# Kernel tuning notes

Hardware: AMD Instinct MI355X
Metric: run time of the kernel (lower is better)

Reference implementation:

```python
import jax, jax.numpy as jnp
import numpy as np


def table_operator(A, B):
    # A, B: (size, batch). Returns (16, size, batch) of soft logic-gate outputs.
    AB = A * B
    A_or_B = A + B - AB
    A_xor_B = A + B - 2.0 * AB
    return jnp.stack([
        jnp.zeros_like(A),          # 0: FALSE
        AB,                         # 1: A AND B
        A - AB,                     # 2: A AND NOT B
        A,                          # 3: A
        B - AB,                     # 4: NOT A AND B
        B,                          # 5: B
        A_xor_B,                    # 6: A XOR B
        A_or_B,                     # 7: A OR B
        1.0 - A_or_B,               # 8: NOR
        1.0 - A_xor_B,              # 9: XNOR
        1.0 - B,                    # 10: NOT B
        1.0 - B + AB,               # 11: B -> A
        1.0 - A,                    # 12: NOT A
        1.0 - A + AB,               # 13: A -> B
        1.0 - AB,                   # 14: NAND
        jnp.ones_like(A),           # 15: TRUE
    ], axis=0)


def setup_inputs() -> dict:
    key = jax.random.key(0)
    k1, k2, k3, k4 = jax.random.split(key, 4)
    prev_size, size, batch = 1024, 1024, 16384
    return {
        "prev_layer_output": jax.random.uniform(k1, (prev_size, batch), jnp.float32),
        "input_A_weights": jax.random.normal(k2, (size, prev_size), jnp.float32),
        "input_B_weights": jax.random.normal(k3, (size, prev_size), jnp.float32),
        "table_weights": jax.random.normal(k4, (16, size), jnp.float32),
    }


def reference(prev_layer_output, input_A_weights, input_B_weights, table_weights):
    # Inference path (torch.is_grad_enabled() == False, drop_out_rate == 0):
    # plain softmaxes, no multiplier shift, no dropout. GradFactor is identity in fwd.
    pA = jax.nn.softmax(input_A_weights, axis=1)   # (size, prev_size)
    pB = jax.nn.softmax(input_B_weights, axis=1)
    pT = jax.nn.softmax(table_weights, axis=0)     # (16, size)
    a = pA @ prev_layer_output                     # (size, batch)
    b = pB @ prev_layer_output                     # (size, batch)
    gates = table_operator(a, b)                   # (16, size, batch)
    return jnp.sum(gates * pT[:, :, None], axis=0)  # (size, batch)
```

## Files before the change

### kernel.cpp

```cpp
#include <hip/hip_runtime.h>
#include <hip/hip_bf16.h>


typedef __attribute__((ext_vector_type(8))) short bf16x8;
typedef __attribute__((ext_vector_type(4))) float f32x4;

__device__ __forceinline__ void gload_lds16(const void* g, void* l) {
    __builtin_amdgcn_global_load_lds(
        (const __attribute__((address_space(1))) void*)g,
        (__attribute__((address_space(3))) void*)l, 16, 0, 0);
}

constexpr int Kp = 1024;
constexpr int Np = 16384;
constexpr int NTB = (Np / 64) * (Kp / 64);

__global__ __launch_bounds__(256) void prep_fused(
    const float* __restrict__ prev, __hip_bfloat16* __restrict__ prevT,
    const float* __restrict__ WA, const float* __restrict__ WB,
    __hip_bfloat16* __restrict__ PA, __hip_bfloat16* __restrict__ PB,
    const float* __restrict__ TW, float4* __restrict__ coef)
{
    const int bid = blockIdx.x;
    const int t = threadIdx.x;

    if (bid < NTB) {
        __shared__ float ls[64][65];
        const int n0 = (bid & 255) * 64;
        const int k0 = (bid >> 8) * 64;
        {
            const int kr = t >> 4, nc = (t & 15) * 4;
            #pragma unroll
            for (int i = 0; i < 4; ++i) {
                const int k = i * 16 + kr;
                float4 v = *(const float4*)&prev[(size_t)(k0 + k) * Np + n0 + nc];
                ls[k][nc + 0] = v.x; ls[k][nc + 1] = v.y;
                ls[k][nc + 2] = v.z; ls[k][nc + 3] = v.w;
            }
        }
        __syncthreads();
        {
            const int n = t >> 2, kc = (t & 3) * 16;
            __align__(16) __hip_bfloat16 tmp[16];
            #pragma unroll
            for (int j = 0; j < 16; ++j) tmp[j] = __float2bfloat16(ls[kc + j][n]);
            __hip_bfloat16* dst = &prevT[(size_t)(n0 + n) * Kp + k0 + kc];
            *(uint4*)(dst + 0) = *(const uint4*)&tmp[0];
            *(uint4*)(dst + 8) = *(const uint4*)&tmp[8];
        }
        return;
    }

    if (bid < NTB + 2048) {
        const int b = bid - NTB;
        const float* W;
        __hip_bfloat16* P;
        if (b < 1024) { W = WA + (size_t)b * Kp;          P = PA + (size_t)b * Kp; }
        else          { W = WB + (size_t)(b - 1024) * Kp; P = PB + (size_t)(b - 1024) * Kp; }

        const int wave = t >> 6, lane = t & 63;
        float4 v = *(const float4*)&W[t * 4];
        float mx = fmaxf(fmaxf(v.x, v.y), fmaxf(v.z, v.w));
        #pragma unroll
        for (int off = 32; off; off >>= 1) mx = fmaxf(mx, __shfl_xor(mx, off));

        __shared__ float redmax[4];
        __shared__ float redsum[4];
        if (lane == 0) redmax[wave] = mx;
        __syncthreads();
        mx = fmaxf(fmaxf(redmax[0], redmax[1]), fmaxf(redmax[2], redmax[3]));

        float e0 = __expf(v.x - mx), e1 = __expf(v.y - mx);
        float e2 = __expf(v.z - mx), e3 = __expf(v.w - mx);
        float s = e0 + e1 + e2 + e3;
        #pragma unroll
        for (int off = 32; off; off >>= 1) s += __shfl_xor(s, off);
        if (lane == 0) redsum[wave] = s;
        __syncthreads();
        s = redsum[0] + redsum[1] + redsum[2] + redsum[3];

        const float inv = 1.0f / s;
        __align__(8) __hip_bfloat16 o[4];
        o[0] = __float2bfloat16(e0 * inv);
        o[1] = __float2bfloat16(e1 * inv);
        o[2] = __float2bfloat16(e2 * inv);
        o[3] = __float2bfloat16(e3 * inv);
        *(uint2*)&P[t * 4] = *(const uint2*)o;
        return;
    }

    const int s = (bid - NTB - 2048) * 256 + t;
    if (s < 1024) {
        float p[16];
        float mx = -1e30f;
        #pragma unroll
        for (int g = 0; g < 16; ++g) { p[g] = TW[g * 1024 + s]; mx = fmaxf(mx, p[g]); }
        float sum = 0.f;
        #pragma unroll
        for (int g = 0; g < 16; ++g) { p[g] = __expf(p[g] - mx); sum += p[g]; }
        const float inv = 1.0f / sum;
        #pragma unroll
        for (int g = 0; g < 16; ++g) p[g] *= inv;
        float w0  = p[8] + p[9] + p[10] + p[11] + p[12] + p[13] + p[14] + p[15];
        float wA  = p[2] + p[3] + p[6] + p[7] - p[8] - p[9] - p[12] - p[13];
        float wB  = p[4] + p[5] + p[6] + p[7] - p[8] - p[9] - p[10] - p[11];
        float wAB = p[1] - p[2] - p[4] - 2.f * p[6] - p[7]
                  + p[8] + 2.f * p[9] + p[11] + p[13] - p[14];
        coef[s] = make_float4(w0, wA, wB, wAB);
    }
}

constexpr int Kd = 1024;
constexpr int Nd = 16384;

__global__ __launch_bounds__(512, 2) void dual_gemm8(
    const __hip_bfloat16* __restrict__ pA,
    const __hip_bfloat16* __restrict__ pB,
    const __hip_bfloat16* __restrict__ prevT,
    const float4* __restrict__ coef,
    float* __restrict__ out)
{
    __shared__ __align__(16) char smem[131072];

    const int t_ = threadIdx.x;
    const int wave = t_ >> 6, lane = t_ & 63;
    const int wr = wave >> 2, wc = wave & 3;
    const int m0 = blockIdx.y * 128;
    const int n0 = blockIdx.x * 256;

    const int fr  = lane & 15;
    const int kg  = lane >> 4;
    const int fsw = fr & 7;
    const int c0 = (kg ^ fsw) * 16;
    const int c1 = ((4 + kg) ^ fsw) * 16;
    const int aoffs = (wr * 128 + fr) * 128;
    const int boffs = 32768 + (wc * 64 + fr) * 128;

    const int sr  = lane >> 3;
    const int swz = ((lane & 7) ^ sr) * 8;
    const int r0  = wave * 16 + sr;
    const __hip_bfloat16* gA0 = pA    + (size_t)(m0 + r0) * Kd + swz;
    const __hip_bfloat16* gA1 = pB    + (size_t)(m0 + r0) * Kd + swz;
    const __hip_bfloat16* gB0 = prevT + (size_t)(n0 + r0) * Kd + swz;
    const __hip_bfloat16* gB1 = prevT + (size_t)(n0 + 128 + r0) * Kd + swz;

    f32x4 acc[8][4] = {};
    bf16x8 aL[8], aH[8], bL[4], bH[4];

#define STG(GP, BB, HOFF, KT) {                                             \
    char* lb = smem + (BB) + (HOFF) + wave * 2048;                          \
    gload_lds16((GP) + (KT), lb);                                           \
    gload_lds16((GP) + (KT) + 8 * Kd, lb + 1024); }

#define RD_AL(BB) _Pragma("unroll") for (int i = 0; i < 4; ++i) {           \
    aL[i*2]   = *(const bf16x8*)(smem + (BB) + aoffs + i * 2048 + c0);      \
    aL[i*2+1] = *(const bf16x8*)(smem + (BB) + aoffs + i * 2048 + c1); }
#define RD_AH(BB) _Pragma("unroll") for (int i = 0; i < 4; ++i) {           \
    aH[i*2]   = *(const bf16x8*)(smem + (BB) + aoffs + 8192 + i * 2048 + c0); \
    aH[i*2+1] = *(const bf16x8*)(smem + (BB) + aoffs + 8192 + i * 2048 + c1); }
#define RD_BL(BB) _Pragma("unroll") for (int j = 0; j < 2; ++j) {           \
    bL[j*2]   = *(const bf16x8*)(smem + (BB) + boffs + j * 2048 + c0);      \
    bL[j*2+1] = *(const bf16x8*)(smem + (BB) + boffs + j * 2048 + c1); }
#define RD_BH(BB) _Pragma("unroll") for (int j = 0; j < 2; ++j) {           \
    bH[j*2]   = *(const bf16x8*)(smem + (BB) + boffs + 4096 + j * 2048 + c0); \
    bH[j*2+1] = *(const bf16x8*)(smem + (BB) + boffs + 4096 + j * 2048 + c1); }

#define VMW(S) asm volatile("s_waitcnt " S ::: "memory")

#define MMQ(AB, BB, I0, J0)                                                 \
    __builtin_amdgcn_s_setprio(1);                                          \
    _Pragma("unroll") for (int i = 0; i < 4; ++i)                           \
    _Pragma("unroll") for (int j = 0; j < 2; ++j)                           \
    _Pragma("unroll") for (int ks = 0; ks < 2; ++ks)                        \
        acc[(I0)+i][(J0)+j] = __builtin_amdgcn_mfma_f32_16x16x32_bf16(      \
            AB[i*2+ks], BB[j*2+ks], acc[(I0)+i][(J0)+j], 0, 0, 0);          \
    __builtin_amdgcn_s_setprio(0);

#define TILE(T, CURB, NXTB, SG, DOTAIL) {                                   \
    if (SG) { STG(gA0, NXTB, 0, ((T)+1)*64)                                 \
              STG(gA1, NXTB, 16384, ((T)+1)*64) }                           \
    RD_BH(CURB)                                                             \
    MMQ(aL, bL, 0, 0)                                                       \
    if (SG) { STG(gB0, NXTB, 32768, ((T)+1)*64) }                           \
    RD_AH(CURB)                                                             \
    MMQ(aL, bH, 0, 2)                                                       \
    if (SG) { STG(gB1, NXTB, 49152, ((T)+1)*64) }                           \
    MMQ(aH, bH, 4, 2)                                                       \
    VMW("vmcnt(0)");                                                        \
    __builtin_amdgcn_s_barrier();                                           \
    __builtin_amdgcn_sched_barrier(0);                                      \
    if (DOTAIL) { RD_AL(NXTB) }                                             \
    MMQ(aH, bL, 4, 0)                                                       \
    if (DOTAIL) { RD_BL(NXTB) }                                             \
}

    STG(gA0, 0, 0,     0)
    STG(gA1, 0, 16384, 0)
    STG(gB0, 0, 32768, 0)
    STG(gB1, 0, 49152, 0)
    VMW("vmcnt(0)");
    __builtin_amdgcn_s_barrier();
    __builtin_amdgcn_sched_barrier(0);
    RD_AL(0) RD_BL(0)

    for (int t = 0; t < 15; ++t) {
        const int cb = (t & 1) << 16;
        TILE(t, cb, cb ^ 65536, 1, 1)
    }
    TILE(15, 65536, 0, 0, 0)

#undef TILE
#undef MMQ
#undef STG
#undef RD_AL
#undef RD_AH
#undef RD_BL
#undef RD_BH
#undef VMW

    __syncthreads();
    if (wr == 1) {
        #pragma unroll
        for (int i = 0; i < 8; ++i) {
            #pragma unroll
            for (int j = 0; j < 4; ++j) {
                const int off = ((((wc * 8 + i) * 4 + j) * 64) + lane) * 16;
                *(f32x4*)(smem + off) = acc[i][j];
            }
        }
    }
    __syncthreads();
    if (wr == 0) {
        const int hi = lane >> 4;
        #pragma unroll
        for (int i = 0; i < 8; ++i) {
            float4 cc[4];
            #pragma unroll
            for (int r = 0; r < 4; ++r) cc[r] = coef[m0 + i * 16 + hi * 4 + r];
            #pragma unroll
            for (int j = 0; j < 4; ++j) {
                const f32x4 bb = *(const f32x4*)(smem + ((((wc * 8 + i) * 4 + j) * 64) + lane) * 16);
                const int n = n0 + wc * 64 + j * 16 + fr;
                #pragma unroll
                for (int r = 0; r < 4; ++r) {
                    const int m = m0 + i * 16 + hi * 4 + r;
                    const float aa = acc[i][j][r];
                    out[(size_t)m * Nd + n] = cc[r].x + cc[r].y * aa + cc[r].z * bb[r]
                                            + cc[r].w * (aa * bb[r]);
                }
            }
        }
    }
}

extern "C" void kernel_launch(void* const* d_in, const int* in_sizes, int n_in,
                              void* d_out, int out_size, void* d_ws, size_t ws_size,
                              hipStream_t stream)
{
    const float* prev = (const float*)d_in[0];
    const float* WA   = (const float*)d_in[1];
    const float* WB   = (const float*)d_in[2];
    const float* TW   = (const float*)d_in[3];
    float* out = (float*)d_out;

    const int size      = in_sizes[3] / 16;
    const int prev_size = in_sizes[1] / size;
    const int batch     = in_sizes[0] / prev_size;

    char* ws = (char*)d_ws;
    __hip_bfloat16* prevT = (__hip_bfloat16*)ws;
    size_t off = (size_t)batch * prev_size * sizeof(__hip_bfloat16);
    __hip_bfloat16* pA = (__hip_bfloat16*)(ws + off);
    off += (size_t)size * prev_size * sizeof(__hip_bfloat16);
    __hip_bfloat16* pB = (__hip_bfloat16*)(ws + off);
    off += (size_t)size * prev_size * sizeof(__hip_bfloat16);
    float4* coef = (float4*)(ws + off);

    const int nprep = (batch / 64) * (prev_size / 64) + 2 * size + (size + 255) / 256;
    prep_fused<<<dim3(nprep), dim3(256), 0, stream>>>(
        prev, prevT, WA, WB, pA, pB, TW, coef);
    dual_gemm8<<<dim3(batch / 256, size / 128), dim3(512), 0, stream>>>(
        pA, pB, prevT, coef, out);
}
```

Measured before the change: 84.53 us.

## Triple-buffer B tiles and prefetch two stages ahead in the dual GEMM

Raises the shared-memory pool to 160KB, with two A buffers and three rotating B buffers. B tiles are now prefetched two K-steps ahead while A stays one step ahead, and the main loop is unrolled into explicit rotations with partial vmcnt waits. LDS reads are moved to the top of each tile, with a barrier and lgkmcnt wait around every MFMA quarter. The aim is to hide global-load latency better, at the cost of many more barriers per tile and a larger LDS footprint.

Measured after the change: 85.32 us. About the same (+0.9%).

```diff
diff --git a/kernel.cpp b/kernel.cpp
--- a/kernel.cpp
+++ b/kernel.cpp
@@ -112,6 +112,8 @@
 
 constexpr int Kd = 1024;
 constexpr int Nd = 16384;
+constexpr int A0_ = 0,     A1_ = 32768;
+constexpr int Q0_ = 65536, Q1_ = 98304, Q2_ = 131072;
 
 __global__ __launch_bounds__(512, 2) void dual_gemm8(
     const __hip_bfloat16* __restrict__ pA,
@@ -120,7 +122,7 @@
     const float4* __restrict__ coef,
     float* __restrict__ out)
 {
-    __shared__ __align__(16) char smem[131072];
+    __shared__ __align__(16) char smem[163840];
 
     const int t_ = threadIdx.x;
     const int wave = t_ >> 6, lane = t_ & 63;
@@ -134,7 +136,7 @@
     const int c0 = (kg ^ fsw) * 16;
     const int c1 = ((4 + kg) ^ fsw) * 16;
     const int aoffs = (wr * 128 + fr) * 128;
-    const int boffs = 32768 + (wc * 64 + fr) * 128;
+    const int boffs = (wc * 64 + fr) * 128;
 
     const int sr  = lane >> 3;
     const int swz = ((lane & 7) ^ sr) * 8;
@@ -165,7 +167,10 @@
     bH[j*2]   = *(const bf16x8*)(smem + (BB) + boffs + 4096 + j * 2048 + c0); \
     bH[j*2+1] = *(const bf16x8*)(smem + (BB) + boffs + 4096 + j * 2048 + c1); }
 
-#define VMW(S) asm volatile("s_waitcnt " S ::: "memory")
+#define VMW(S)  asm volatile("s_waitcnt " S ::: "memory")
+#define LGK(S)  asm volatile("s_waitcnt " S ::: "memory")
+#define BAR     __builtin_amdgcn_s_barrier()
+#define SBR     __builtin_amdgcn_sched_barrier(0)
 
 #define MMQ(AB, BB, I0, J0)                                                 \
     __builtin_amdgcn_s_setprio(1);                                          \
@@ -173,42 +178,54 @@
     _Pragma("unroll") for (int j = 0; j < 2; ++j)                           \
     _Pragma("unroll") for (int ks = 0; ks < 2; ++ks)                        \
         acc[(I0)+i][(J0)+j] = __builtin_amdgcn_mfma_f32_16x16x32_bf16(      \
-            AB[i*2+ks], BB[j*2+ks], acc[(I0)+i][(J0)+j], 0, 0, 0);          \
+            AB[i*2+ks], BB[(J0 ? 0 : 0)+j*2+ks], acc[(I0)+i][(J0)+j], 0,0,0); \
     __builtin_amdgcn_s_setprio(0);
 
-#define TILE(T, CURB, NXTB, SG, DOTAIL) {                                   \
-    if (SG) { STG(gA0, NXTB, 0, ((T)+1)*64)                                 \
-              STG(gA1, NXTB, 16384, ((T)+1)*64) }                           \
-    RD_BH(CURB)                                                             \
-    MMQ(aL, bL, 0, 0)                                                       \
-    if (SG) { STG(gB0, NXTB, 32768, ((T)+1)*64) }                           \
-    RD_AH(CURB)                                                             \
-    MMQ(aL, bH, 0, 2)                                                       \
-    if (SG) { STG(gB1, NXTB, 49152, ((T)+1)*64) }                           \
-    MMQ(aH, bH, 4, 2)                                                       \
-    VMW("vmcnt(0)");                                                        \
-    __builtin_amdgcn_s_barrier();                                           \
-    __builtin_amdgcn_sched_barrier(0);                                      \
-    if (DOTAIL) { RD_AL(NXTB) }                                             \
-    MMQ(aH, bL, 4, 0)                                                       \
-    if (DOTAIL) { RD_BL(NXTB) }                                             \
-}
-
-    STG(gA0, 0, 0,     0)
-    STG(gA1, 0, 16384, 0)
-    STG(gB0, 0, 32768, 0)
-    STG(gB1, 0, 49152, 0)
-    VMW("vmcnt(0)");
-    __builtin_amdgcn_s_barrier();
-    __builtin_amdgcn_sched_barrier(0);
-    RD_AL(0) RD_BL(0)
-
-    for (int t = 0; t < 15; ++t) {
-        const int cb = (t & 1) << 16;
-        TILE(t, cb, cb ^ 65536, 1, 1)
-    }
-    TILE(15, 65536, 0, 0, 0)
-
+#define TILE(T, CA, CB, NA, B2, SGA, SGB, DOVM, VMSTR) {                    \
+    RD_AL(CA) RD_BL(CB)                                                     \
+    if (SGA) STG(gA0, NA, 0, ((T)+1)*64)                                    \
+    LGK("lgkmcnt(8)");                                                      \
+    BAR; LGK("lgkmcnt(0)"); SBR;                                            \
+    MMQ(aL, bL, 0, 0) BAR;                                                  \
+    RD_BH(CB)                                                               \
+    if (SGA) STG(gA1, NA, 16384, ((T)+1)*64)                                \
+    BAR; LGK("lgkmcnt(0)"); SBR;                                            \
+    MMQ(aL, bH, 0, 2) BAR;                                                  \
+    RD_AH(CA)                                                               \
+    if (SGB) STG(gB0, B2, 0, ((T)+2)*64)                                    \
+    BAR; LGK("lgkmcnt(0)"); SBR;                                            \
+    MMQ(aH, bH, 4, 2) BAR;                                                  \
+    if (SGB) STG(gB1, B2, 16384, ((T)+2)*64)                                \
+    if (DOVM) VMW(VMSTR);                                                   \
+    BAR; SBR;                                                               \
+    MMQ(aH, bL, 4, 0) BAR;                                                  \
+}
+
+    STG(gB0, Q0_, 0,     0)
+    STG(gB1, Q0_, 16384, 0)
+    STG(gA0, A0_, 0,     0)
+    STG(gA1, A0_, 16384, 0)
+    STG(gB0, Q1_, 0,     64)
+    STG(gB1, Q1_, 16384, 64)
+    VMW("vmcnt(4)");
+    BAR; SBR;
+
+#define SIX(TB)                                                             \
+    TILE((TB)+0, A0_, Q0_, A1_, Q2_, 1, 1, 1, "vmcnt(4)")                   \
+    TILE((TB)+1, A1_, Q1_, A0_, Q0_, 1, 1, 1, "vmcnt(4)")                   \
+    TILE((TB)+2, A0_, Q2_, A1_, Q1_, 1, 1, 1, "vmcnt(4)")                   \
+    TILE((TB)+3, A1_, Q0_, A0_, Q2_, 1, 1, 1, "vmcnt(4)")                   \
+    TILE((TB)+4, A0_, Q1_, A1_, Q0_, 1, 1, 1, "vmcnt(4)")                   \
+    TILE((TB)+5, A1_, Q2_, A0_, Q1_, 1, 1, 1, "vmcnt(4)")
+
+    SIX(0)
+    SIX(6)
+    TILE(12, A0_, Q0_, A1_, Q2_, 1, 1, 1, "vmcnt(4)")
+    TILE(13, A1_, Q1_, A0_, Q0_, 1, 1, 1, "vmcnt(4)")
+    TILE(14, A0_, Q2_, A1_, Q0_, 1, 0, 1, "vmcnt(0)")
+    TILE(15, A1_, Q0_, A0_, Q0_, 0, 0, 0, "vmcnt(0)")
+
+#undef SIX
 #undef TILE
 #undef MMQ
 #undef STG
@@ -217,6 +234,9 @@
 #undef RD_BL
 #undef RD_BH
 #undef VMW
+#undef LGK
+#undef BAR
+#undef SBR
 
     __syncthreads();
     if (wr == 1) {
```
